# Kernel optimization log

Hardware: AMD Instinct MI355X
Metric: run time of the kernel (lower is better)

## Reference

```python
import jax, jax.numpy as jnp
import numpy as np

NUM_EXPERTS = 64
TOP_K = 2
CAPACITY_FACTOR = 1.25
D_MODEL = 2048
BATCH, SEQ = 4, 4096


def setup_inputs() -> dict:
    key = jax.random.key(0)
    kx, kw = jax.random.split(key)
    x = jax.random.normal(kx, (BATCH, SEQ, D_MODEL), dtype=jnp.float32)
    # router weight: Linear(input_dim, num_experts, bias=False), init std=0.001
    W = jax.random.normal(kw, (NUM_EXPERTS, D_MODEL), dtype=jnp.float32) * 0.001
    return {"x": x, "W": W}


def reference(x, W):
    B, S, D = x.shape
    N = B * S  # combined batch of tokens
    E = NUM_EXPERTS
    k = TOP_K
    capacity = int(CAPACITY_FACTOR * N * k / E)  # static Python int

    x_flat = x.reshape(N, D)
    router_logits = jnp.einsum('nd,ed->ne', x_flat, W)  # [N, E]
    routing_weights = jax.nn.softmax(router_logits, axis=-1)

    top_k_weights, top_k_indices = jax.lax.top_k(routing_weights, k)  # [N, k]
    top_k_weights = top_k_weights / (top_k_weights.sum(-1, keepdims=True) + 1e-8)

    expert_counts = jnp.zeros((E,), dtype=jnp.float32)
    dispatch_mask = jnp.zeros((N, E), dtype=jnp.float32)
    token_ids = jnp.arange(N)

    # Sequential over k (fixed, small): within a k-step the capacity check uses
    # counts from previous steps only, matching the torch scatter semantics.
    for k_idx in range(k):
        expert_idx = top_k_indices[:, k_idx]            # [N]
        under_cap = expert_counts[expert_idx] < capacity  # [N] bool
        expert_counts = expert_counts + jax.ops.segment_sum(
            under_cap.astype(jnp.float32), expert_idx, num_segments=E)
        # top-k experts are distinct per token, so add == set on zero-init slots
        dispatch_mask = dispatch_mask.at[token_ids, expert_idx].add(
            jnp.where(under_cap, top_k_weights[:, k_idx], 0.0))

    # Tokens that got dropped everywhere go to the least-loaded expert with w=1
    unrouted = dispatch_mask.sum(-1) == 0                     # [N]
    least_loaded = jnp.argmax(capacity - expert_counts)       # scalar
    dispatch_mask = jnp.where(
        unrouted[:, None] & (jnp.arange(E)[None, :] == least_loaded),
        1.0, dispatch_mask)

    normalized_dispatch_mask = dispatch_mask / (dispatch_mask.sum(-1, keepdims=True) + 1e-8)

    router_z_loss = jnp.mean(jnp.square(router_logits))
    counts = normalized_dispatch_mask.sum(0)                  # [E]
    target_count = float(N * k / E)
    load_balance_loss = jnp.mean(jnp.square(counts / float(N) - target_count / float(N)))
    router_loss = 0.001 * jax.lax.stop_gradient(router_z_loss) \
                + 0.001 * jax.lax.stop_gradient(load_balance_loss)

    return (jax.lax.stop_gradient(routing_weights), normalized_dispatch_mask, router_loss)
```

## Files before the change

### kernel.cpp

```cpp
#include <hip/hip_runtime.h>
#include <hip/hip_bf16.h>
#include <math.h>

#define N_TOK 16384
#define D_MODEL 2048
#define N_EXP 64
#define CAPACITY 640
#define KSPLIT 4
#define KSLICE (D_MODEL / KSPLIT)
#define BK 32
#define XP 36
#define NREP 8

__global__ __launch_bounds__(256, 4) void k1_gemm(
    const float* __restrict__ x, const float* __restrict__ W,
    float* __restrict__ part) {
  __shared__ float xs[64][XP];
  __shared__ float ws[BK][N_EXP];

  const int t = threadIdx.x;
  const int ks = blockIdx.x >> 8;
  const int grp = blockIdx.x & 255;
  const int m0 = grp * 64;
  const int kb = ks * KSLICE;

  const int tr = t >> 4;
  const int tc = t & 15;
  const int xr = t >> 2;
  const int xc = (t & 3) * 8;
  const int we = t & 63;
  const int wc = (t >> 6) * 8;

  const float* xg = x + (size_t)(m0 + xr) * D_MODEL + kb + xc;
  const float* wg = W + (size_t)we * D_MODEL + kb + wc;

  float4 xp0 = *(const float4*)xg, xp1 = *(const float4*)(xg + 4);
  float4 wp0 = *(const float4*)wg, wp1 = *(const float4*)(wg + 4);

  float acc[4][4] = {};

  for (int s = 0; s < KSLICE / BK; s++) {
    __syncthreads();
    *(float4*)&xs[xr][xc] = xp0;
    *(float4*)&xs[xr][xc + 4] = xp1;
    ws[wc + 0][we] = wp0.x; ws[wc + 1][we] = wp0.y;
    ws[wc + 2][we] = wp0.z; ws[wc + 3][we] = wp0.w;
    ws[wc + 4][we] = wp1.x; ws[wc + 5][we] = wp1.y;
    ws[wc + 6][we] = wp1.z; ws[wc + 7][we] = wp1.w;
    __syncthreads();
    if (s + 1 < KSLICE / BK) {
      const int d = (s + 1) * BK;
      xp0 = *(const float4*)(xg + d); xp1 = *(const float4*)(xg + d + 4);
      wp0 = *(const float4*)(wg + d); wp1 = *(const float4*)(wg + d + 4);
    }
#pragma unroll
    for (int k4 = 0; k4 < BK / 4; k4++) {
      float4 a[4], w4[4];
#pragma unroll
      for (int i = 0; i < 4; i++)
        a[i] = *(const float4*)&xs[tr + 16 * i][k4 * 4];
#pragma unroll
      for (int kk = 0; kk < 4; kk++)
        w4[kk] = *(const float4*)&ws[k4 * 4 + kk][tc * 4];
#pragma unroll
      for (int kk = 0; kk < 4; kk++)
#pragma unroll
        for (int i = 0; i < 4; i++) {
          const float av = (&a[i].x)[kk];
          acc[i][0] = fmaf(av, w4[kk].x, acc[i][0]);
          acc[i][1] = fmaf(av, w4[kk].y, acc[i][1]);
          acc[i][2] = fmaf(av, w4[kk].z, acc[i][2]);
          acc[i][3] = fmaf(av, w4[kk].w, acc[i][3]);
        }
    }
  }
#pragma unroll
  for (int i = 0; i < 4; i++) {
    float* pp = part + ((size_t)ks * N_TOK + m0 + tr + 16 * i) * N_EXP + tc * 4;
    *(float4*)pp = make_float4(acc[i][0], acc[i][1], acc[i][2], acc[i][3]);
  }
}

__global__ __launch_bounds__(256) void k2_softmax(
    const float* __restrict__ part, float* __restrict__ rw_out,
    int2* __restrict__ top12, float2* __restrict__ wts,
    int* __restrict__ histR, float* __restrict__ zR) {
  __shared__ float zred[4];
  const int lane = threadIdx.x & 63;
  const int wid = threadIdx.x >> 6;
  const int n = blockIdx.x * 4 + wid;
  const int rep = blockIdx.x & (NREP - 1);

  float v = 0.f;
#pragma unroll
  for (int s = 0; s < KSPLIT; s++)
    v += part[((size_t)s * N_TOK + n) * N_EXP + lane];

  float zp = v * v;
#pragma unroll
  for (int off = 32; off; off >>= 1) zp += __shfl_xor(zp, off);

  float m = v;
#pragma unroll
  for (int off = 32; off; off >>= 1) m = fmaxf(m, __shfl_xor(m, off));
  float p = __expf(v - m);
  float ssum = p;
#pragma unroll
  for (int off = 32; off; off >>= 1) ssum += __shfl_xor(ssum, off);
  const float rw = p / ssum;
  rw_out[(size_t)n * N_EXP + lane] = rw;

  const unsigned long long b1 = __ballot(v == m);
  const int i1 = __builtin_ctzll(b1);
  float v2 = (lane == i1) ? -INFINITY : v;
#pragma unroll
  for (int off = 32; off; off >>= 1) v2 = fmaxf(v2, __shfl_xor(v2, off));
  const unsigned long long b2 = __ballot(v == v2) & ~(1ull << i1);
  const int i2 = __builtin_ctzll(b2);

  const float rw1 = __shfl(rw, i1);
  const float rw2 = __shfl(rw, i2);
  if (lane == 0) {
    const float denom = rw1 + rw2 + 1e-8f;
    top12[n] = make_int2(i1, i2);
    wts[n] = make_float2(rw1 / denom, rw2 / denom);
    atomicAdd(&histR[(rep * N_EXP + i1) * 16], 1);
    zred[wid] = zp;
  }
  __syncthreads();
  if (threadIdx.x == 0)
    atomicAdd(&zR[rep * 16], zred[0] + zred[1] + zred[2] + zred[3]);
}

__global__ __launch_bounds__(256) void k3_dispatch(
    const int2* __restrict__ top12, const float2* __restrict__ wts,
    const int* __restrict__ histR, float* __restrict__ mask_out,
    float* __restrict__ cntR) {
  const int lane = threadIdx.x & 63;
  const int wid = threadIdx.x >> 6;
  const int n = blockIdx.x * 4 + wid;
  const int rep = blockIdx.x & (NREP - 1);

  const int2 ij = top12[n];
  const float2 w = wts[n];
  int h = 0;
#pragma unroll
  for (int r = 0; r < NREP; r++) h += histR[(r * N_EXP + ij.y) * 16];
  const bool allowed = h < CAPACITY;
  const float ssum = w.x + (allowed ? w.y : 0.f);
  const float inv = 1.f / (ssum + 1e-8f);
  float val = 0.f;
  if (lane == ij.x) val = w.x * inv;
  else if (allowed && lane == ij.y) val = w.y * inv;
  mask_out[(size_t)n * N_EXP + lane] = val;
  if (val != 0.f) atomicAdd(&cntR[(rep * N_EXP + lane) * 16], val);
}

__global__ void k4_loss(const float* __restrict__ cntR,
                        const float* __restrict__ zR,
                        float* __restrict__ loss_out) {
  const int lane = threadIdx.x;
  float c = 0.f;
#pragma unroll
  for (int r = 0; r < NREP; r++) c += cntR[(r * N_EXP + lane) * 16];
  const float d = (c - 512.0f) * (1.0f / 16384.0f);
  float v = d * d;
#pragma unroll
  for (int off = 32; off; off >>= 1) v += __shfl_xor(v, off);
  if (lane == 0) {
    float z = 0.f;
#pragma unroll
    for (int r = 0; r < NREP; r++) z += zR[r * 16];
    const float lb = v * (1.0f / 64.0f);
    loss_out[0] = 0.001f * (z * (1.0f / (16384.0f * 64.0f))) + 0.001f * lb;
  }
}

extern "C" void kernel_launch(void* const* d_in, const int* in_sizes, int n_in,
                              void* d_out, int out_size, void* d_ws, size_t ws_size,
                              hipStream_t stream) {
  const float* x = (const float*)d_in[0];
  const float* W = (const float*)d_in[1];
  float* out = (float*)d_out;
  float* rw_out = out;
  float* mask_out = out + (size_t)N_TOK * N_EXP;
  float* loss_out = out + 2 * (size_t)N_TOK * N_EXP;

  char* ws = (char*)d_ws;
  float* part = (float*)ws;
  int* histR = (int*)(ws + 16777216);
  float* cntR = (float*)(ws + 16777216 + 32768);
  float* zR = (float*)(ws + 16777216 + 65536);
  int2* top12 = (int2*)(ws + 16777216 + 131072);
  float2* wts = (float2*)(ws + 16777216 + 262144);

  hipMemsetAsync(histR, 0, 65536 + 512, stream);
  k1_gemm<<<KSPLIT * 256, 256, 0, stream>>>(x, W, part);
  k2_softmax<<<N_TOK / 4, 256, 0, stream>>>(part, rw_out, top12, wts, histR, zR);
  k3_dispatch<<<N_TOK / 4, 256, 0, stream>>>(top12, wts, histR, mask_out, cntR);
  k4_loss<<<1, 64, 0, stream>>>(cntR, zR, loss_out);
}
```

Before: 238.6 us.

## Drop LDS tiling in router GEMM; read transposed W directly from global/cache

```diff
diff --git a/kernel.cpp b/kernel.cpp
--- a/kernel.cpp
+++ b/kernel.cpp
@@ -8,16 +8,23 @@
 #define CAPACITY 640
 #define KSPLIT 4
 #define KSLICE (D_MODEL / KSPLIT)
-#define BK 32
-#define XP 36
 #define NREP 8
 
+__global__ __launch_bounds__(256) void k0_transpose(
+    const float* __restrict__ W, float* __restrict__ Wt) {
+  const int tid = blockIdx.x * 256 + threadIdx.x;
+  const int e = tid >> 9;
+  const int k4 = tid & 511;
+  const float4 v = *(const float4*)(W + (size_t)e * D_MODEL + 4 * k4);
+  Wt[(size_t)(4 * k4 + 0) * N_EXP + e] = v.x;
+  Wt[(size_t)(4 * k4 + 1) * N_EXP + e] = v.y;
+  Wt[(size_t)(4 * k4 + 2) * N_EXP + e] = v.z;
+  Wt[(size_t)(4 * k4 + 3) * N_EXP + e] = v.w;
+}
+
 __global__ __launch_bounds__(256, 4) void k1_gemm(
-    const float* __restrict__ x, const float* __restrict__ W,
+    const float* __restrict__ x, const float* __restrict__ Wt,
     float* __restrict__ part) {
-  __shared__ float xs[64][XP];
-  __shared__ float ws[BK][N_EXP];
-
   const int t = threadIdx.x;
   const int ks = blockIdx.x >> 8;
   const int grp = blockIdx.x & 255;
@@ -26,54 +33,48 @@
 
   const int tr = t >> 4;
   const int tc = t & 15;
-  const int xr = t >> 2;
-  const int xc = (t & 3) * 8;
-  const int we = t & 63;
-  const int wc = (t >> 6) * 8;
-
-  const float* xg = x + (size_t)(m0 + xr) * D_MODEL + kb + xc;
-  const float* wg = W + (size_t)we * D_MODEL + kb + wc;
-
-  float4 xp0 = *(const float4*)xg, xp1 = *(const float4*)(xg + 4);
-  float4 wp0 = *(const float4*)wg, wp1 = *(const float4*)(wg + 4);
+
+  const float* xg = x + (size_t)(m0 + tr) * D_MODEL + kb;
+  const float* wg = Wt + (size_t)kb * N_EXP + tc * 4;
 
   float acc[4][4] = {};
 
-  for (int s = 0; s < KSLICE / BK; s++) {
-    __syncthreads();
-    *(float4*)&xs[xr][xc] = xp0;
-    *(float4*)&xs[xr][xc + 4] = xp1;
-    ws[wc + 0][we] = wp0.x; ws[wc + 1][we] = wp0.y;
-    ws[wc + 2][we] = wp0.z; ws[wc + 3][we] = wp0.w;
-    ws[wc + 4][we] = wp1.x; ws[wc + 5][we] = wp1.y;
-    ws[wc + 6][we] = wp1.z; ws[wc + 7][we] = wp1.w;
-    __syncthreads();
-    if (s + 1 < KSLICE / BK) {
-      const int d = (s + 1) * BK;
-      xp0 = *(const float4*)(xg + d); xp1 = *(const float4*)(xg + d + 4);
-      wp0 = *(const float4*)(wg + d); wp1 = *(const float4*)(wg + d + 4);
-    }
-#pragma unroll
-    for (int k4 = 0; k4 < BK / 4; k4++) {
-      float4 a[4], w4[4];
-#pragma unroll
-      for (int i = 0; i < 4; i++)
-        a[i] = *(const float4*)&xs[tr + 16 * i][k4 * 4];
-#pragma unroll
-      for (int kk = 0; kk < 4; kk++)
-        w4[kk] = *(const float4*)&ws[k4 * 4 + kk][tc * 4];
-#pragma unroll
-      for (int kk = 0; kk < 4; kk++)
-#pragma unroll
-        for (int i = 0; i < 4; i++) {
-          const float av = (&a[i].x)[kk];
-          acc[i][0] = fmaf(av, w4[kk].x, acc[i][0]);
-          acc[i][1] = fmaf(av, w4[kk].y, acc[i][1]);
-          acc[i][2] = fmaf(av, w4[kk].z, acc[i][2]);
-          acc[i][3] = fmaf(av, w4[kk].w, acc[i][3]);
-        }
-    }
-  }
+  for (int k4 = 0; k4 < KSLICE / 4; k4++) {
+    float4 a0 = *(const float4*)(xg + (size_t)0 * 16 * D_MODEL + 4 * k4);
+    float4 a1 = *(const float4*)(xg + (size_t)1 * 16 * D_MODEL + 4 * k4);
+    float4 a2 = *(const float4*)(xg + (size_t)2 * 16 * D_MODEL + 4 * k4);
+    float4 a3 = *(const float4*)(xg + (size_t)3 * 16 * D_MODEL + 4 * k4);
+    float4 w0 = *(const float4*)(wg + (size_t)(4 * k4 + 0) * N_EXP);
+    float4 w1 = *(const float4*)(wg + (size_t)(4 * k4 + 1) * N_EXP);
+    float4 w2 = *(const float4*)(wg + (size_t)(4 * k4 + 2) * N_EXP);
+    float4 w3 = *(const float4*)(wg + (size_t)(4 * k4 + 3) * N_EXP);
+#define FMA_STEP(AV, WV)                         \
+    acc[AV][0] = fmaf(a##AV.x, w0.x, acc[AV][0]);
+#undef FMA_STEP
+#define ROW(i, av)                                   \
+    acc[i][0] = fmaf(av, wq.x, acc[i][0]);           \
+    acc[i][1] = fmaf(av, wq.y, acc[i][1]);           \
+    acc[i][2] = fmaf(av, wq.z, acc[i][2]);           \
+    acc[i][3] = fmaf(av, wq.w, acc[i][3]);
+    {
+      float4 wq = w0;
+      ROW(0, a0.x) ROW(1, a1.x) ROW(2, a2.x) ROW(3, a3.x)
+    }
+    {
+      float4 wq = w1;
+      ROW(0, a0.y) ROW(1, a1.y) ROW(2, a2.y) ROW(3, a3.y)
+    }
+    {
+      float4 wq = w2;
+      ROW(0, a0.z) ROW(1, a1.z) ROW(2, a2.z) ROW(3, a3.z)
+    }
+    {
+      float4 wq = w3;
+      ROW(0, a0.w) ROW(1, a1.w) ROW(2, a2.w) ROW(3, a3.w)
+    }
+#undef ROW
+  }
+
 #pragma unroll
   for (int i = 0; i < 4; i++) {
     float* pp = part + ((size_t)ks * N_TOK + m0 + tr + 16 * i) * N_EXP + tc * 4;
@@ -188,14 +189,16 @@
 
   char* ws = (char*)d_ws;
   float* part = (float*)ws;
-  int* histR = (int*)(ws + 16777216);
-  float* cntR = (float*)(ws + 16777216 + 32768);
-  float* zR = (float*)(ws + 16777216 + 65536);
-  int2* top12 = (int2*)(ws + 16777216 + 131072);
-  float2* wts = (float2*)(ws + 16777216 + 262144);
+  float* Wt = (float*)(ws + 16777216);
+  int* histR = (int*)(ws + 17301504);
+  float* cntR = (float*)(ws + 17301504 + 32768);
+  float* zR = (float*)(ws + 17301504 + 65536);
+  int2* top12 = (int2*)(ws + 17301504 + 131072);
+  float2* wts = (float2*)(ws + 17301504 + 262144);
 
   hipMemsetAsync(histR, 0, 65536 + 512, stream);
-  k1_gemm<<<KSPLIT * 256, 256, 0, stream>>>(x, W, part);
+  k0_transpose<<<128, 256, 0, stream>>>(W, Wt);
+  k1_gemm<<<KSPLIT * 256, 256, 0, stream>>>(x, Wt, part);
   k2_softmax<<<N_TOK / 4, 256, 0, stream>>>(part, rw_out, top12, wts, histR, zR);
   k3_dispatch<<<N_TOK / 4, 256, 0, stream>>>(top12, wts, histR, mask_out, cntR);
   k4_loss<<<1, 64, 0, stream>>>(cntR, zR, loss_out);
```

Measured after the change: 337.7 us. 41.5% more time.
